# Kernel tuning notes

Measured on AMD Instinct MI355X. Metric: run time of the kernel, lower is better.

The kernel has to match this reference:

```python
import jax, jax.numpy as jnp
import numpy as np

HIDDEN_DIM = 512  # global scale divisor used in the original layer


def setup_inputs() -> dict:
    key = jax.random.key(0)
    k1, k2 = jax.random.split(key)
    B, S, H = 32, 8192, 512
    states_h = jax.random.normal(k1, (B, H), dtype=jnp.float32)
    enc_out = jax.random.normal(k2, (B, S, H), dtype=jnp.float32)
    return {"states_h": states_h, "enc_out": enc_out}


def reference(states_h, enc_out):
    # align_score = matmul(enc_out, dec_h^T) / hidden_dim -> [B, S, 1]
    align = jnp.einsum("bsh,bh->bs", enc_out, states_h) / HIDDEN_DIM
    # softmax over the sequence axis (axis=1 in the original [B,S,1] tensor)
    weights = jax.nn.softmax(align, axis=1)[:, :, None]           # [B, S, 1]
    # context = sum_s enc_out * weights -> [B, H], then expand to [B, 1, H]
    context = jnp.einsum("bsh,bs->bh", enc_out, weights[:, :, 0])
    context = context[:, None, :]                                  # [B, 1, H]
    return (context, weights)
```

## Files before the change

### kernel.cpp

```cpp
#include <hip/hip_runtime.h>
#include <hip/hip_bf16.h>
#include <math.h>


#define BB 32
#define SS 8192
#define HH 512
#define RPW 64
#define NP (SS / RPW)
#define ITERS (RPW / 4)

__global__ __launch_bounds__(64) void attn_pass1(
    const float* __restrict__ states, const float* __restrict__ enc,
    float* __restrict__ align, float* __restrict__ pl, float* __restrict__ pC)
{
    const int blk  = blockIdx.x;
    const int b    = blk >> 7;
    const int p    = blk & (NP - 1);
    const int lane = threadIdx.x;
    const int g    = lane >> 4;
    const int s    = lane & 15;

    const float4* st4 = (const float4*)(states + (size_t)b * HH);
    float4 sh[8];
    #pragma unroll
    for (int k = 0; k < 8; ++k) sh[k] = st4[k * 16 + s];

    const float* rowbase = enc + ((size_t)b * SS + (size_t)p * RPW) * HH;

    float4 ctx[8];
    #pragma unroll
    for (int k = 0; k < 8; ++k) ctx[k] = make_float4(0.f, 0.f, 0.f, 0.f);
    float lsum = 0.0f;
    float my_a = 0.0f;

    #pragma unroll 2
    for (int it = 0; it < ITERS; ++it) {
        const float4* rp = (const float4*)(rowbase + (size_t)(it * 4 + g) * HH);
        float4 e[8];
        #pragma unroll
        for (int k = 0; k < 8; ++k) e[k] = rp[k * 16 + s];

        float d0 = 0.f, d1 = 0.f, d2 = 0.f, d3 = 0.f;
        #pragma unroll
        for (int k = 0; k < 2; ++k) {
            d0 = fmaf(e[k].x, sh[k].x, fmaf(e[k].y, sh[k].y, fmaf(e[k].z, sh[k].z, fmaf(e[k].w, sh[k].w, d0))));
            d1 = fmaf(e[k+2].x, sh[k+2].x, fmaf(e[k+2].y, sh[k+2].y, fmaf(e[k+2].z, sh[k+2].z, fmaf(e[k+2].w, sh[k+2].w, d1))));
            d2 = fmaf(e[k+4].x, sh[k+4].x, fmaf(e[k+4].y, sh[k+4].y, fmaf(e[k+4].z, sh[k+4].z, fmaf(e[k+4].w, sh[k+4].w, d2))));
            d3 = fmaf(e[k+6].x, sh[k+6].x, fmaf(e[k+6].y, sh[k+6].y, fmaf(e[k+6].z, sh[k+6].z, fmaf(e[k+6].w, sh[k+6].w, d3))));
        }
        float d = (d0 + d1) + (d2 + d3);

        #pragma unroll
        for (int mask = 1; mask < 16; mask <<= 1)
            d += __shfl_xor(d, mask, 64);

        float a = d * (1.0f / 512.0f);
        if (s == it) my_a = a;
        float pr = __expf(a);
        lsum += pr;

        #pragma unroll
        for (int k = 0; k < 8; ++k) {
            ctx[k].x = fmaf(pr, e[k].x, ctx[k].x);
            ctx[k].y = fmaf(pr, e[k].y, ctx[k].y);
            ctx[k].z = fmaf(pr, e[k].z, ctx[k].z);
            ctx[k].w = fmaf(pr, e[k].w, ctx[k].w);
        }
    }

    align[(size_t)b * SS + (size_t)p * RPW + s * 4 + g] = my_a;

    #pragma unroll
    for (int mask = 16; mask < 64; mask <<= 1) {
        lsum += __shfl_xor(lsum, mask, 64);
        #pragma unroll
        for (int k = 0; k < 8; ++k) {
            ctx[k].x += __shfl_xor(ctx[k].x, mask, 64);
            ctx[k].y += __shfl_xor(ctx[k].y, mask, 64);
            ctx[k].z += __shfl_xor(ctx[k].z, mask, 64);
            ctx[k].w += __shfl_xor(ctx[k].w, mask, 64);
        }
    }

    if (lane == 0) pl[b * NP + p] = lsum;

    float4* Cp = (float4*)(pC + (size_t)(b * NP + p) * HH);
    Cp[(2 * g)     * 16 + s] = ctx[2 * g];
    Cp[(2 * g + 1) * 16 + s] = ctx[2 * g + 1];
}

__global__ __launch_bounds__(256) void attn_pass2(
    const float* __restrict__ align, const float* __restrict__ pl,
    const float* __restrict__ pC, float* __restrict__ out_ctx,
    float* __restrict__ out_w)
{
    const int b     = blockIdx.x / 10;
    const int slice = blockIdx.x % 10;
    const int t     = threadIdx.x;

    __shared__ float sL[2];
    if (t < NP) {
        float v = pl[b * NP + t];
        #pragma unroll
        for (int mask = 1; mask < 64; mask <<= 1)
            v += __shfl_xor(v, mask, 64);
        if ((t & 63) == 0) sL[t >> 6] = v;
    }
    __syncthreads();
    const float invL = 1.0f / (sL[0] + sL[1]);

    if (slice < 2) {
        const int h = slice * 256 + t;
        const float* Cb = pC + (size_t)b * NP * HH + h;
        float acc = 0.0f;
        #pragma unroll 8
        for (int p = 0; p < NP; ++p)
            acc += Cb[(size_t)p * HH];
        out_ctx[b * HH + h] = acc * invL;
    } else {
        const int s0 = (slice - 2) * 1024;
        const float* al = align + (size_t)b * SS + s0;
        float*       ow = out_w + (size_t)b * SS + s0;
        #pragma unroll
        for (int i = 0; i < 4; ++i)
            ow[t + i * 256] = __expf(al[t + i * 256]) * invL;
    }
}

extern "C" void kernel_launch(void* const* d_in, const int* in_sizes, int n_in,
                              void* d_out, int out_size, void* d_ws, size_t ws_size,
                              hipStream_t stream) {
    const float* states = (const float*)d_in[0];
    const float* enc    = (const float*)d_in[1];

    float* out_ctx = (float*)d_out;
    float* out_w   = (float*)d_out + (size_t)BB * HH;

    float* ws_align = (float*)d_ws;
    float* ws_pl    = ws_align + (size_t)BB * SS;
    float* ws_pC    = ws_pl    + (size_t)BB * NP;

    attn_pass1<<<BB * NP, 64, 0, stream>>>(states, enc, ws_align, ws_pl, ws_pC);
    attn_pass2<<<BB * 10, 256, 0, stream>>>(ws_align, ws_pl, ws_pC, out_ctx, out_w);
}
```

Before: 710.9 us.

## Restructure pass1 into 256-thread blocks with per-wave 16-row chunks and register prefetch

Pass1 now launches 4096 blocks of 4 waves, each wave handling 16 rows. Each row is spread across the whole wave, so the dot product uses a full 64-lane shuffle reduction. Rows are loaded four at a time with software-pipelined double buffering in registers, and per-thread context state drops to two float4s, which lowers register pressure. The cost is 4x more partial context vectors (NP=512) written to and reread from workspace, so pass2's reduction gets longer; pass2 splits it over four accumulators.

```diff
diff --git a/kernel.cpp b/kernel.cpp
--- a/kernel.cpp
+++ b/kernel.cpp
@@ -6,88 +6,78 @@
 #define BB 32
 #define SS 8192
 #define HH 512
-#define RPW 64
-#define NP (SS / RPW)
-#define ITERS (RPW / 4)
+#define CPB 128
+#define RPW 16
+#define NP 512
 
-__global__ __launch_bounds__(64) void attn_pass1(
+__global__ __launch_bounds__(256, 4) void attn_pass1(
     const float* __restrict__ states, const float* __restrict__ enc,
     float* __restrict__ align, float* __restrict__ pl, float* __restrict__ pC)
 {
     const int blk  = blockIdx.x;
     const int b    = blk >> 7;
-    const int p    = blk & (NP - 1);
-    const int lane = threadIdx.x;
-    const int g    = lane >> 4;
-    const int s    = lane & 15;
+    const int c    = blk & 127;
+    const int lane = threadIdx.x & 63;
+    const int wv   = threadIdx.x >> 6;
+    const int p    = (c << 2) | wv;
 
     const float4* st4 = (const float4*)(states + (size_t)b * HH);
-    float4 sh[8];
+    const float4 sh0 = st4[lane];
+    const float4 sh1 = st4[lane + 64];
+
+    const float4* rp = (const float4*)(enc + ((size_t)b * SS + (size_t)p * RPW) * HH);
+
+    float4 ctx0 = make_float4(0.f,0.f,0.f,0.f);
+    float4 ctx1 = make_float4(0.f,0.f,0.f,0.f);
+    float  lsum = 0.0f, my_a = 0.0f;
+
+    float4 cur0[4], cur1[4], nxt0[4], nxt1[4];
     #pragma unroll
-    for (int k = 0; k < 8; ++k) sh[k] = st4[k * 16 + s];
-
-    const float* rowbase = enc + ((size_t)b * SS + (size_t)p * RPW) * HH;
-
-    float4 ctx[8];
-    #pragma unroll
-    for (int k = 0; k < 8; ++k) ctx[k] = make_float4(0.f, 0.f, 0.f, 0.f);
-    float lsum = 0.0f;
-    float my_a = 0.0f;
-
-    #pragma unroll 2
-    for (int it = 0; it < ITERS; ++it) {
-        const float4* rp = (const float4*)(rowbase + (size_t)(it * 4 + g) * HH);
-        float4 e[8];
-        #pragma unroll
-        for (int k = 0; k < 8; ++k) e[k] = rp[k * 16 + s];
-
-        float d0 = 0.f, d1 = 0.f, d2 = 0.f, d3 = 0.f;
-        #pragma unroll
-        for (int k = 0; k < 2; ++k) {
-            d0 = fmaf(e[k].x, sh[k].x, fmaf(e[k].y, sh[k].y, fmaf(e[k].z, sh[k].z, fmaf(e[k].w, sh[k].w, d0))));
-            d1 = fmaf(e[k+2].x, sh[k+2].x, fmaf(e[k+2].y, sh[k+2].y, fmaf(e[k+2].z, sh[k+2].z, fmaf(e[k+2].w, sh[k+2].w, d1))));
-            d2 = fmaf(e[k+4].x, sh[k+4].x, fmaf(e[k+4].y, sh[k+4].y, fmaf(e[k+4].z, sh[k+4].z, fmaf(e[k+4].w, sh[k+4].w, d2))));
-            d3 = fmaf(e[k+6].x, sh[k+6].x, fmaf(e[k+6].y, sh[k+6].y, fmaf(e[k+6].z, sh[k+6].z, fmaf(e[k+6].w, sh[k+6].w, d3))));
-        }
-        float d = (d0 + d1) + (d2 + d3);
-
-        #pragma unroll
-        for (int mask = 1; mask < 16; mask <<= 1)
-            d += __shfl_xor(d, mask, 64);
-
-        float a = d * (1.0f / 512.0f);
-        if (s == it) my_a = a;
-        float pr = __expf(a);
-        lsum += pr;
-
-        #pragma unroll
-        for (int k = 0; k < 8; ++k) {
-            ctx[k].x = fmaf(pr, e[k].x, ctx[k].x);
-            ctx[k].y = fmaf(pr, e[k].y, ctx[k].y);
-            ctx[k].z = fmaf(pr, e[k].z, ctx[k].z);
-            ctx[k].w = fmaf(pr, e[k].w, ctx[k].w);
-        }
+    for (int r = 0; r < 4; ++r) {
+        cur0[r] = rp[r * 128 + lane];
+        cur1[r] = rp[r * 128 + 64 + lane];
     }
 
-    align[(size_t)b * SS + (size_t)p * RPW + s * 4 + g] = my_a;
-
     #pragma unroll
-    for (int mask = 16; mask < 64; mask <<= 1) {
-        lsum += __shfl_xor(lsum, mask, 64);
+    for (int it = 0; it < 4; ++it) {
+        if (it < 3) {
+            #pragma unroll
+            for (int r = 0; r < 4; ++r) {
+                nxt0[r] = rp[(it * 4 + 4 + r) * 128 + lane];
+                nxt1[r] = rp[(it * 4 + 4 + r) * 128 + 64 + lane];
+            }
+        }
         #pragma unroll
-        for (int k = 0; k < 8; ++k) {
-            ctx[k].x += __shfl_xor(ctx[k].x, mask, 64);
-            ctx[k].y += __shfl_xor(ctx[k].y, mask, 64);
-            ctx[k].z += __shfl_xor(ctx[k].z, mask, 64);
-            ctx[k].w += __shfl_xor(ctx[k].w, mask, 64);
+        for (int r = 0; r < 4; ++r) {
+            const float4 e0 = cur0[r], e1 = cur1[r];
+            float d = e0.x*sh0.x + e0.y*sh0.y + e0.z*sh0.z + e0.w*sh0.w
+                    + e1.x*sh1.x + e1.y*sh1.y + e1.z*sh1.z + e1.w*sh1.w;
+            #pragma unroll
+            for (int mask = 1; mask < 64; mask <<= 1)
+                d += __shfl_xor(d, mask, 64);
+            const float a = d * (1.0f / 512.0f);
+            const int row = it * 4 + r;
+            if (lane == row) my_a = a;
+            const float pr = __expf(a);
+            lsum += pr;
+            ctx0.x = fmaf(pr, e0.x, ctx0.x);
+            ctx0.y = fmaf(pr, e0.y, ctx0.y);
+            ctx0.z = fmaf(pr, e0.z, ctx0.z);
+            ctx0.w = fmaf(pr, e0.w, ctx0.w);
+            ctx1.x = fmaf(pr, e1.x, ctx1.x);
+            ctx1.y = fmaf(pr, e1.y, ctx1.y);
+            ctx1.z = fmaf(pr, e1.z, ctx1.z);
+            ctx1.w = fmaf(pr, e1.w, ctx1.w);
         }
+        #pragma unroll
+        for (int r = 0; r < 4; ++r) { cur0[r] = nxt0[r]; cur1[r] = nxt1[r]; }
     }
 
-    if (lane == 0) pl[b * NP + p] = lsum;
-
-    float4* Cp = (float4*)(pC + (size_t)(b * NP + p) * HH);
-    Cp[(2 * g)     * 16 + s] = ctx[2 * g];
-    Cp[(2 * g + 1) * 16 + s] = ctx[2 * g + 1];
+    if (lane < RPW) align[(size_t)b * SS + (size_t)p * RPW + lane] = my_a;
+    if (lane == 0)  pl[b * NP + p] = lsum;
+    float4* Cp = (float4*)(pC + ((size_t)b * NP + p) * HH);
+    Cp[lane]      = ctx0;
+    Cp[lane + 64] = ctx1;
 }
 
 __global__ __launch_bounds__(256) void attn_pass2(
@@ -99,25 +89,27 @@
     const int slice = blockIdx.x % 10;
     const int t     = threadIdx.x;
 
-    __shared__ float sL[2];
-    if (t < NP) {
-        float v = pl[b * NP + t];
-        #pragma unroll
-        for (int mask = 1; mask < 64; mask <<= 1)
-            v += __shfl_xor(v, mask, 64);
-        if ((t & 63) == 0) sL[t >> 6] = v;
-    }
+    __shared__ float sred[4];
+    float v = pl[b * NP + t] + pl[b * NP + 256 + t];
+    #pragma unroll
+    for (int mask = 1; mask < 64; mask <<= 1)
+        v += __shfl_xor(v, mask, 64);
+    if ((t & 63) == 0) sred[t >> 6] = v;
     __syncthreads();
-    const float invL = 1.0f / (sL[0] + sL[1]);
+    const float invL = 1.0f / (sred[0] + sred[1] + sred[2] + sred[3]);
 
     if (slice < 2) {
-        const int h = slice * 256 + t;
+        const int h = (slice << 8) + t;
         const float* Cb = pC + (size_t)b * NP * HH + h;
-        float acc = 0.0f;
-        #pragma unroll 8
-        for (int p = 0; p < NP; ++p)
-            acc += Cb[(size_t)p * HH];
-        out_ctx[b * HH + h] = acc * invL;
+        float a0 = 0.f, a1 = 0.f, a2 = 0.f, a3 = 0.f;
+        #pragma unroll 4
+        for (int pp = 0; pp < NP; pp += 4) {
+            a0 += Cb[(size_t)(pp + 0) * HH];
+            a1 += Cb[(size_t)(pp + 1) * HH];
+            a2 += Cb[(size_t)(pp + 2) * HH];
+            a3 += Cb[(size_t)(pp + 3) * HH];
+        }
+        out_ctx[b * HH + h] = (a0 + a1 + a2 + a3) * invL;
     } else {
         const int s0 = (slice - 2) * 1024;
         const float* al = align + (size_t)b * SS + s0;
@@ -141,6 +133,6 @@
     float* ws_pl    = ws_align + (size_t)BB * SS;
     float* ws_pC    = ws_pl    + (size_t)BB * NP;
 
-    attn_pass1<<<BB * NP, 64, 0, stream>>>(states, enc, ws_align, ws_pl, ws_pC);
+    attn_pass1<<<BB * CPB, 256, 0, stream>>>(states, enc, ws_align, ws_pl, ws_pC);
     attn_pass2<<<BB * 10, 256, 0, stream>>>(ws_align, ws_pl, ws_pC, out_ctx, out_w);
 }
```

New measurement: 740.8 us. +4.2%, slower.
